# Kernel optimization log

Measured on AMD Instinct MI355X. Metric: run time of the kernel, lower is better.

## Reference

```python
import jax, jax.numpy as jnp
import numpy as np

N_NODES = 50000
N_EDGES = 800000
IN_FEAT = 4
HIDDEN = 128
NUM_LAYERS = 3


def setup_inputs() -> dict:
    key = jax.random.key(0)
    ks = jax.random.split(key, 16)
    x = jax.random.normal(ks[0], (N_NODES, IN_FEAT), dtype=jnp.float32)
    edge_index = jax.random.randint(ks[1], (2, N_EDGES), 0, N_NODES, dtype=jnp.int64)

    def lin(k, fan_in, fan_out):
        bound = 1.0 / np.sqrt(fan_in)
        k1, k2 = jax.random.split(k)
        W = jax.random.uniform(k1, (fan_in, fan_out), minval=-bound, maxval=bound, dtype=jnp.float32)
        b = jax.random.uniform(k2, (fan_out,), minval=-bound, maxval=bound, dtype=jnp.float32)
        return W, b

    W_enc, b_enc = lin(ks[2], IN_FEAT, HIDDEN)
    W_g1, b_g1 = lin(ks[3], HIDDEN, HIDDEN)
    W_g2, b_g2 = lin(ks[4], HIDDEN, HIDDEN)
    W_g3, b_g3 = lin(ks[5], HIDDEN, HIDDEN)
    W_m1, b_m1 = lin(ks[6], 2 * HIDDEN, HIDDEN)
    W_m2, b_m2 = lin(ks[7], HIDDEN, 3)
    return {
        "x": x, "edge_index": edge_index,
        "W_enc": W_enc, "b_enc": b_enc,
        "W_g1": W_g1, "b_g1": b_g1,
        "W_g2": W_g2, "b_g2": b_g2,
        "W_g3": W_g3, "b_g3": b_g3,
        "W_m1": W_m1, "b_m1": b_m1,
        "W_m2": W_m2, "b_m2": b_m2,
    }


def _gcn_forward(x, edge_index, W_enc, b_enc, gcn_params, W_m1, b_m1, W_m2, b_m2):
    n = x.shape[0]
    # Node encoder (linear + ReLU) -> [N, H]
    h = jax.nn.relu(x @ W_enc + b_enc)

    # Add self-loops once (GCNConv default add_self_loops=True)
    src = jnp.concatenate([edge_index[0], jnp.arange(n, dtype=edge_index.dtype)])
    dst = jnp.concatenate([edge_index[1], jnp.arange(n, dtype=edge_index.dtype)])
    # Symmetric degree normalization: D^{-1/2} (A+I) D^{-1/2}
    deg = jax.ops.segment_sum(jnp.ones_like(dst, dtype=h.dtype), dst, num_segments=n)
    deg_inv_sqrt = jnp.where(deg > 0, jax.lax.rsqrt(jnp.maximum(deg, 1.0)), 0.0)
    norm = (deg_inv_sqrt[src] * deg_inv_sqrt[dst])[:, None]  # [E+N, 1]

    for (W, b) in gcn_params:
        m = (h @ W)[src] * norm                       # gather + scale messages
        h = jax.ops.segment_sum(m, dst, num_segments=n) + b
        h = jax.nn.relu(h)                            # dropout is identity at eval

    # Edge classifier: gather endpoints, concat, MLP -> [E, 3]
    ef = jnp.concatenate([h[edge_index[0]], h[edge_index[1]]], axis=-1)
    return jax.nn.relu(ef @ W_m1 + b_m1) @ W_m2 + b_m2


def reference(x, edge_index, W_enc, b_enc, W_g1, b_g1, W_g2, b_g2, W_g3, b_g3, W_m1, b_m1, W_m2, b_m2):
    gcn_params = [(W_g1, b_g1), (W_g2, b_g2), (W_g3, b_g3)]
    return _gcn_forward(x, edge_index, W_enc, b_enc, gcn_params, W_m1, b_m1, W_m2, b_m2)
```

## Files before the change

kernel.cpp:

```cpp
#include <hip/hip_runtime.h>
#include <hip/hip_bf16.h>

#define N_NODES 50000
#define N_EDGES 800000
#define HID 128
#define NBUCKET 1024
#define N_NODE_BLOCKS ((N_NODES + 255) / 256)

typedef __attribute__((ext_vector_type(8))) short bf16x8;
typedef __attribute__((ext_vector_type(4))) float f32x4;

__device__ __forceinline__ ushort f2bf(float f) {
    uint u = __float_as_uint(f);
    return (ushort)((u + 0x7FFFu + ((u >> 16) & 1u)) >> 16);
}
__device__ __forceinline__ float bf2f(ushort h) { return __uint_as_float(((uint)h) << 16); }

__global__ void k_count(const int* __restrict__ ei, int* cnt) {
    int e = blockIdx.x * blockDim.x + threadIdx.x;
    if (e < N_EDGES) atomicAdd(&cnt[ei[N_EDGES + e]], 1);
}

__global__ __launch_bounds__(256) void k_bhist(const int* __restrict__ cnt, int* gHist,
                                               int* __restrict__ blockBase) {
    __shared__ int lh[NBUCKET];
    int t = threadIdx.x;
    for (int d = t; d < NBUCKET; d += 256) lh[d] = 0;
    __syncthreads();
    int n = blockIdx.x * 256 + t;
    if (n < N_NODES) {
        int deg = min(cnt[n], NBUCKET - 1);
        atomicAdd(&lh[deg], 1);
    }
    __syncthreads();
    for (int d = t; d < NBUCKET; d += 256) {
        int c = lh[d];
        blockBase[blockIdx.x * NBUCKET + d] = c ? atomicAdd(&gHist[d], c) : 0;
    }
}

__global__ __launch_bounds__(NBUCKET) void k_prefix(const int* __restrict__ gHist,
                                                    int* __restrict__ histBase,
                                                    int* __restrict__ edgeBase,
                                                    int* __restrict__ rowStartP) {
    __shared__ int a[NBUCKET];
    __shared__ int b[NBUCKET];
    int t = threadIdx.x;
    int h = gHist[t];
    a[t] = h;
    b[t] = h * t;
    __syncthreads();
    for (int off = 1; off < NBUCKET; off <<= 1) {
        int av = (t >= off) ? a[t - off] : 0;
        int bv = (t >= off) ? b[t - off] : 0;
        __syncthreads();
        a[t] += av;
        b[t] += bv;
        __syncthreads();
    }
    histBase[t] = a[t] - h;
    edgeBase[t] = b[t] - h * t;
    if (t == 0) rowStartP[N_NODES] = N_EDGES;
}

__global__ __launch_bounds__(256) void k_rank(const int* __restrict__ cnt,
                                              const int* __restrict__ histBase,
                                              const int* __restrict__ edgeBase,
                                              const int* __restrict__ blockBase,
                                              int* __restrict__ rank,
                                              int* __restrict__ rowStartP,
                                              float* __restrict__ dinvP) {
    __shared__ int cur[NBUCKET];
    int t = threadIdx.x;
    for (int d = t; d < NBUCKET; d += 256) cur[d] = 0;
    __syncthreads();
    int n = blockIdx.x * 256 + t;
    if (n < N_NODES) {
        int deg = min(cnt[n], NBUCKET - 1);
        int slot = atomicAdd(&cur[deg], 1);
        int r = histBase[deg] + blockBase[blockIdx.x * NBUCKET + deg] + slot;
        rank[n] = r;
        rowStartP[r] = edgeBase[deg] + (r - histBase[deg]) * deg;
        dinvP[r] = rsqrtf(1.0f + (float)deg);
    }
}

__global__ void k_fill(const int* __restrict__ ei, const int* __restrict__ rank,
                       const int* __restrict__ rowStartP, int* cursorP,
                       int2* __restrict__ csrE) {
    int e = blockIdx.x * blockDim.x + threadIdx.x;
    if (e < N_EDGES) {
        int s = ei[e];
        int d = ei[N_EDGES + e];
        int rd = rank[d];
        int pos = rowStartP[rd] + atomicAdd(&cursorP[rd], 1);
        csrE[pos] = make_int2(rank[s], e);
    }
}

struct WSplitArgs {
    const float* src[5];
    ushort* th[5];
    ushort* tl[5];
};

__global__ void k_tsplit5(WSplitArgs a) {
    int i = blockIdx.x * 256 + threadIdx.x;
    int which = i >> 14, r = i & 16383;
    int k = r >> 7, j = r & 127;
    float v = a.src[which][r];
    ushort hi = f2bf(v);
    a.th[which][j * 128 + k] = hi;
    a.tl[which][j * 128 + k] = f2bf(v - bf2f(hi));
}

__global__ void k_encoder(const float* __restrict__ x, const float* __restrict__ W,
                          const float* __restrict__ b, const int* __restrict__ rank,
                          ushort* __restrict__ hH, ushort* __restrict__ hL) {
    int i = blockIdx.x * 256 + threadIdx.x;
    int n = i >> 6, l = i & 63;
    int j = l * 2;
    float4 xv = *(const float4*)(x + (size_t)n * 4);
    float2 acc = *(const float2*)(b + j);
    float2 w0 = *(const float2*)(W + 0 * 128 + j);
    float2 w1 = *(const float2*)(W + 1 * 128 + j);
    float2 w2 = *(const float2*)(W + 2 * 128 + j);
    float2 w3 = *(const float2*)(W + 3 * 128 + j);
    acc.x += xv.x * w0.x + xv.y * w1.x + xv.z * w2.x + xv.w * w3.x;
    acc.y += xv.x * w0.y + xv.y * w1.y + xv.z * w2.y + xv.w * w3.y;
    float v0 = fmaxf(acc.x, 0.f), v1 = fmaxf(acc.y, 0.f);
    ushort h0 = f2bf(v0), h1 = f2bf(v1);
    ushort l0 = f2bf(v0 - bf2f(h0)), l1 = f2bf(v1 - bf2f(h1));
    size_t o = (size_t)rank[n] * 64 + l;
    ((uint*)hH)[o] = (uint)h0 | ((uint)h1 << 16);
    ((uint*)hL)[o] = (uint)l0 | ((uint)l1 << 16);
}

__global__ __launch_bounds__(256) void k_gemm_mfma(const ushort* __restrict__ AH,
                                                   const ushort* __restrict__ AL,
                                                   const ushort* __restrict__ BTH,
                                                   const ushort* __restrict__ BTL,
                                                   float* __restrict__ out,
                                                   const float* __restrict__ scale, int M) {
    int tid = threadIdx.x;
    int w = tid >> 6, l = tid & 63;
    int ln = l & 15, lk = l >> 4;
    int r0 = blockIdx.x * 128 + w * 32;
    int row0 = r0 + ln, row1 = r0 + 16 + ln;
    int a0 = row0 < M ? row0 : M - 1;
    int a1 = row1 < M ? row1 : M - 1;

    f32x4 acc0[8] = {};
    f32x4 acc1[8] = {};
#pragma unroll
    for (int kc = 0; kc < 4; ++kc) {
        int ko = kc * 32 + lk * 8;
        bf16x8 h0H = *(const bf16x8*)(AH + (size_t)a0 * 128 + ko);
        bf16x8 h0L = *(const bf16x8*)(AL + (size_t)a0 * 128 + ko);
        bf16x8 h1H = *(const bf16x8*)(AH + (size_t)a1 * 128 + ko);
        bf16x8 h1L = *(const bf16x8*)(AL + (size_t)a1 * 128 + ko);
#pragma unroll
        for (int nt = 0; nt < 8; ++nt) {
            size_t boff = (size_t)(nt * 16 + ln) * 128 + ko;
            bf16x8 wH = *(const bf16x8*)(BTH + boff);
            bf16x8 wL = *(const bf16x8*)(BTL + boff);
            acc0[nt] = __builtin_amdgcn_mfma_f32_16x16x32_bf16(wH, h0H, acc0[nt], 0, 0, 0);
            acc0[nt] = __builtin_amdgcn_mfma_f32_16x16x32_bf16(wL, h0H, acc0[nt], 0, 0, 0);
            acc0[nt] = __builtin_amdgcn_mfma_f32_16x16x32_bf16(wH, h0L, acc0[nt], 0, 0, 0);
            acc1[nt] = __builtin_amdgcn_mfma_f32_16x16x32_bf16(wH, h1H, acc1[nt], 0, 0, 0);
            acc1[nt] = __builtin_amdgcn_mfma_f32_16x16x32_bf16(wL, h1H, acc1[nt], 0, 0, 0);
            acc1[nt] = __builtin_amdgcn_mfma_f32_16x16x32_bf16(wH, h1L, acc1[nt], 0, 0, 0);
        }
    }
    float s0v = scale[a0];
    float s1v = scale[a1];
#pragma unroll
    for (int nt = 0; nt < 8; ++nt) {
        int jb = nt * 16 + lk * 4;
        if (row0 < M) {
            *(float4*)(out + (size_t)row0 * 128 + jb) =
                make_float4(acc0[nt][0] * s0v, acc0[nt][1] * s0v, acc0[nt][2] * s0v, acc0[nt][3] * s0v);
        }
        if (row1 < M) {
            *(float4*)(out + (size_t)row1 * 128 + jb) =
                make_float4(acc1[nt][0] * s1v, acc1[nt][1] * s1v, acc1[nt][2] * s1v, acc1[nt][3] * s1v);
        }
    }
}

__global__ __launch_bounds__(512, 8) void k_agg_gemm(
    const float* __restrict__ hw, const float* __restrict__ bg,
    const float* __restrict__ dinvP, const int* __restrict__ rowStartP,
    const int2* __restrict__ csrE,
    const ushort* __restrict__ BTH1, const ushort* __restrict__ BTL1,
    const ushort* __restrict__ BTH2, const ushort* __restrict__ BTL2,
    float* __restrict__ out1, float* __restrict__ out2,
    const float* __restrict__ b1, const float* __restrict__ outScale) {
    __shared__ uint AsH[16][68];
    __shared__ uint AsL[16][68];
    int tid = threadIdx.x;
    int w = tid >> 6, l = tid & 63;
    int sub = l >> 5;
    int g2 = (l >> 4) & 1;
    int li = l & 15;
    int c8 = li * 8;
    int n = blockIdx.x * 16 + w * 2 + sub;

    float4 aA, aB;
    if (g2 == 0) {
        aA = *(const float4*)(hw + (size_t)n * 128 + c8);
        aB = *(const float4*)(hw + (size_t)n * 128 + c8 + 4);
    } else {
        aA = make_float4(0.f, 0.f, 0.f, 0.f);
        aB = aA;
    }
    int s0 = rowStartP[n], s1 = rowStartP[n + 1];
    int k = s0 + g2;
    float4 v0a = make_float4(0.f, 0.f, 0.f, 0.f), v0b = v0a;
    if (k < s1) {
        const float* r = hw + (size_t)csrE[k].x * 128 + c8;
        v0a = *(const float4*)(r);
        v0b = *(const float4*)(r + 4);
    }
    for (; k < s1; k += 2) {
        float4 v1a = make_float4(0.f, 0.f, 0.f, 0.f), v1b = v1a;
        if (k + 2 < s1) {
            const float* r = hw + (size_t)csrE[k + 2].x * 128 + c8;
            v1a = *(const float4*)(r);
            v1b = *(const float4*)(r + 4);
        }
        aA.x += v0a.x; aA.y += v0a.y; aA.z += v0a.z; aA.w += v0a.w;
        aB.x += v0b.x; aB.y += v0b.y; aB.z += v0b.z; aB.w += v0b.w;
        v0a = v1a;
        v0b = v1b;
    }
    aA.x += __shfl_xor(aA.x, 16); aA.y += __shfl_xor(aA.y, 16);
    aA.z += __shfl_xor(aA.z, 16); aA.w += __shfl_xor(aA.w, 16);
    aB.x += __shfl_xor(aB.x, 16); aB.y += __shfl_xor(aB.y, 16);
    aB.z += __shfl_xor(aB.z, 16); aB.w += __shfl_xor(aB.w, 16);

    if (g2 == 0) {
        float di = dinvP[n];
        float4 bbA = *(const float4*)(bg + c8);
        float4 bbB = *(const float4*)(bg + c8 + 4);
        float f0 = fmaxf(bbA.x + di * aA.x, 0.f);
        float f1 = fmaxf(bbA.y + di * aA.y, 0.f);
        float f2 = fmaxf(bbA.z + di * aA.z, 0.f);
        float f3 = fmaxf(bbA.w + di * aA.w, 0.f);
        float f4 = fmaxf(bbB.x + di * aB.x, 0.f);
        float f5 = fmaxf(bbB.y + di * aB.y, 0.f);
        float f6 = fmaxf(bbB.z + di * aB.z, 0.f);
        float f7 = fmaxf(bbB.w + di * aB.w, 0.f);
        ushort h0 = f2bf(f0), h1 = f2bf(f1), h2 = f2bf(f2), h3 = f2bf(f3);
        ushort h4 = f2bf(f4), h5 = f2bf(f5), h6 = f2bf(f6), h7 = f2bf(f7);
        uint4 uh = make_uint4((uint)h0 | ((uint)h1 << 16), (uint)h2 | ((uint)h3 << 16),
                              (uint)h4 | ((uint)h5 << 16), (uint)h6 | ((uint)h7 << 16));
        ushort l0 = f2bf(f0 - bf2f(h0)), l1 = f2bf(f1 - bf2f(h1));
        ushort l2 = f2bf(f2 - bf2f(h2)), l3 = f2bf(f3 - bf2f(h3));
        ushort l4 = f2bf(f4 - bf2f(h4)), l5 = f2bf(f5 - bf2f(h5));
        ushort l6 = f2bf(f6 - bf2f(h6)), l7 = f2bf(f7 - bf2f(h7));
        uint4 ul = make_uint4((uint)l0 | ((uint)l1 << 16), (uint)l2 | ((uint)l3 << 16),
                              (uint)l4 | ((uint)l5 << 16), (uint)l6 | ((uint)l7 << 16));
        int r = w * 2 + sub;
        *(uint4*)&AsH[r][li * 4] = uh;
        *(uint4*)&AsL[r][li * 4] = ul;
    }
    __syncthreads();

    int ln = l & 15, lk = l >> 4;
    int ct = w;
    int node = blockIdx.x * 16 + ln;
    f32x4 acc1 = {};
    f32x4 acc2 = {};
#pragma unroll
    for (int kc = 0; kc < 4; ++kc) {
        uint4 uh = *(uint4*)&AsH[ln][kc * 16 + lk * 4];
        uint4 ul = *(uint4*)&AsL[ln][kc * 16 + lk * 4];
        bf16x8 hh, hl;
        __builtin_memcpy(&hh, &uh, 16);
        __builtin_memcpy(&hl, &ul, 16);
        size_t boff = (size_t)(ct * 16 + ln) * 128 + kc * 32 + lk * 8;
        bf16x8 wh = *(const bf16x8*)(BTH1 + boff);
        bf16x8 wl = *(const bf16x8*)(BTL1 + boff);
        acc1 = __builtin_amdgcn_mfma_f32_16x16x32_bf16(wh, hh, acc1, 0, 0, 0);
        acc1 = __builtin_amdgcn_mfma_f32_16x16x32_bf16(wl, hh, acc1, 0, 0, 0);
        acc1 = __builtin_amdgcn_mfma_f32_16x16x32_bf16(wh, hl, acc1, 0, 0, 0);
        if (BTH2) {
            bf16x8 wh2 = *(const bf16x8*)(BTH2 + boff);
            bf16x8 wl2 = *(const bf16x8*)(BTL2 + boff);
            acc2 = __builtin_amdgcn_mfma_f32_16x16x32_bf16(wh2, hh, acc2, 0, 0, 0);
            acc2 = __builtin_amdgcn_mfma_f32_16x16x32_bf16(wl2, hh, acc2, 0, 0, 0);
            acc2 = __builtin_amdgcn_mfma_f32_16x16x32_bf16(wh2, hl, acc2, 0, 0, 0);
        }
    }
    int jb = ct * 16 + lk * 4;
    if (outScale) {
        float s = outScale[node];
        *(float4*)(out1 + (size_t)node * 128 + jb) =
            make_float4(acc1[0] * s, acc1[1] * s, acc1[2] * s, acc1[3] * s);
    } else {
        *(float4*)(out1 + (size_t)node * 128 + jb) =
            make_float4(acc1[0], acc1[1], acc1[2], acc1[3]);
        float4 bv = *(const float4*)(b1 + jb);
        *(float4*)(out2 + (size_t)node * 128 + jb) =
            make_float4(acc2[0] + bv.x, acc2[1] + bv.y, acc2[2] + bv.z, acc2[3] + bv.w);
    }
}

__global__ __launch_bounds__(256) void k_edge_final(const float* __restrict__ P,
                                                    const float* __restrict__ Qb,
                                                    const int* __restrict__ rowStartP,
                                                    const int2* __restrict__ csrE,
                                                    const float* __restrict__ W2,
                                                    const float* __restrict__ b2,
                                                    float* __restrict__ out) {
    int wid = (blockIdx.x * 256 + threadIdx.x) >> 6;
    int l = threadIdx.x & 63;
    if (wid >= N_NODES) return;
    int s0 = rowStartP[wid], s1 = rowStartP[wid + 1];
    if (s0 >= s1) return;
    int j8 = (l & 15) * 8;
    int g = l >> 4;

    float4 qa = *(const float4*)(Qb + (size_t)wid * 128 + j8);
    float4 qb = *(const float4*)(Qb + (size_t)wid * 128 + j8 + 4);
    float w2r[8][3];
#pragma unroll
    for (int k = 0; k < 8; ++k) {
        w2r[k][0] = W2[(j8 + k) * 3 + 0];
        w2r[k][1] = W2[(j8 + k) * 3 + 1];
        w2r[k][2] = W2[(j8 + k) * 3 + 2];
    }
    float bz0 = b2[0], bz1 = b2[1], bz2 = b2[2];

    int k = s0 + g;
    int2 c = make_int2(0, 0);
    float4 pa = make_float4(0.f, 0.f, 0.f, 0.f), pb = pa;
    if (k < s1) {
        c = csrE[k];
        const float* pr = P + (size_t)c.x * 128 + j8;
        pa = *(const float4*)(pr);
        pb = *(const float4*)(pr + 4);
    }
    for (; k < s1; k += 4) {
        int kn = k + 4;
        int2 cn = make_int2(0, 0);
        float4 pan = make_float4(0.f, 0.f, 0.f, 0.f), pbn = pan;
        if (kn < s1) {
            cn = csrE[kn];
            const float* prn = P + (size_t)cn.x * 128 + j8;
            pan = *(const float4*)(prn);
            pbn = *(const float4*)(prn + 4);
        }
        float z[8];
        z[0] = fmaxf(pa.x + qa.x, 0.f);
        z[1] = fmaxf(pa.y + qa.y, 0.f);
        z[2] = fmaxf(pa.z + qa.z, 0.f);
        z[3] = fmaxf(pa.w + qa.w, 0.f);
        z[4] = fmaxf(pb.x + qb.x, 0.f);
        z[5] = fmaxf(pb.y + qb.y, 0.f);
        z[6] = fmaxf(pb.z + qb.z, 0.f);
        z[7] = fmaxf(pb.w + qb.w, 0.f);
        float o0 = 0.f, o1 = 0.f, o2 = 0.f;
#pragma unroll
        for (int q = 0; q < 8; ++q) {
            o0 += z[q] * w2r[q][0];
            o1 += z[q] * w2r[q][1];
            o2 += z[q] * w2r[q][2];
        }
#pragma unroll
        for (int m = 1; m < 16; m <<= 1) {
            o0 += __shfl_xor(o0, m);
            o1 += __shfl_xor(o1, m);
            o2 += __shfl_xor(o2, m);
        }
        if ((l & 15) == 0) {
            float* op = out + (size_t)c.y * 3;
            op[0] = o0 + bz0;
            op[1] = o1 + bz1;
            op[2] = o2 + bz2;
        }
        c = cn;
        pa = pan;
        pb = pbn;
    }
}

extern "C" void kernel_launch(void* const* d_in, const int* in_sizes, int n_in,
                              void* d_out, int out_size, void* d_ws, size_t ws_size,
                              hipStream_t stream) {
    const float* x     = (const float*)d_in[0];
    const int*   ei    = (const int*)d_in[1];
    const float* W_enc = (const float*)d_in[2];
    const float* b_enc = (const float*)d_in[3];
    const float* Wg[3] = {(const float*)d_in[4], (const float*)d_in[6], (const float*)d_in[8]};
    const float* bg[3] = {(const float*)d_in[5], (const float*)d_in[7], (const float*)d_in[9]};
    const float* W_m1  = (const float*)d_in[10];
    const float* b_m1  = (const float*)d_in[11];
    const float* W_m2  = (const float*)d_in[12];
    const float* b_m2  = (const float*)d_in[13];
    float* out = (float*)d_out;

    char* w = (char*)d_ws;
    ushort* hH      = (ushort*)w;  w += (size_t)N_NODES * HID * 2;
    ushort* hL      = (ushort*)w;  w += (size_t)N_NODES * HID * 2;
    float*  bufA    = (float*)w;   w += (size_t)N_NODES * HID * 4;
    float*  bufB    = (float*)w;   w += (size_t)N_NODES * HID * 4;
    int2*   csrE    = (int2*)w;    w += (size_t)N_EDGES * 8;
    int*    cnt     = (int*)w;     w += (size_t)N_NODES * 4;
    int*    cursorP = (int*)w;     w += (size_t)N_NODES * 4;
    int*    gHist   = (int*)w;     w += NBUCKET * 4;
    size_t  zeroBytes = (size_t)(N_NODES * 2 + NBUCKET) * 4;
    int*    rank    = (int*)w;     w += (size_t)N_NODES * 4;
    int*    rowStartP = (int*)w;   w += (size_t)(N_NODES + 4) * 4;
    float*  dinvP   = (float*)w;   w += (size_t)N_NODES * 4;
    int*    histBase = (int*)w;    w += NBUCKET * 4;
    int*    edgeBase = (int*)w;    w += NBUCKET * 4;
    int*    blockBase = (int*)w;   w += (size_t)N_NODE_BLOCKS * NBUCKET * 4;
    ushort* WgTH[3], *WgTL[3];
    for (int i = 0; i < 3; ++i) {
        WgTH[i] = (ushort*)w; w += 128 * 128 * 2;
        WgTL[i] = (ushort*)w; w += 128 * 128 * 2;
    }
    ushort* WtTH = (ushort*)w; w += 128 * 128 * 2;
    ushort* WtTL = (ushort*)w; w += 128 * 128 * 2;
    ushort* WbTH = (ushort*)w; w += 128 * 128 * 2;
    ushort* WbTL = (ushort*)w; w += 128 * 128 * 2;

    float* P  = (float*)hH;
    float* Qb = bufB;

    hipMemsetAsync(cnt, 0, zeroBytes, stream);
    k_count<<<(N_EDGES + 255) / 256, 256, 0, stream>>>(ei, cnt);
    k_bhist<<<N_NODE_BLOCKS, 256, 0, stream>>>(cnt, gHist, blockBase);
    k_prefix<<<1, NBUCKET, 0, stream>>>(gHist, histBase, edgeBase, rowStartP);
    k_rank<<<N_NODE_BLOCKS, 256, 0, stream>>>(cnt, histBase, edgeBase, blockBase,
                                              rank, rowStartP, dinvP);
    k_fill<<<(N_EDGES + 255) / 256, 256, 0, stream>>>(ei, rank, rowStartP, cursorP, csrE);

    WSplitArgs wa;
    wa.src[0] = Wg[0]; wa.th[0] = WgTH[0]; wa.tl[0] = WgTL[0];
    wa.src[1] = Wg[1]; wa.th[1] = WgTH[1]; wa.tl[1] = WgTL[1];
    wa.src[2] = Wg[2]; wa.th[2] = WgTH[2]; wa.tl[2] = WgTL[2];
    wa.src[3] = W_m1;             wa.th[3] = WtTH; wa.tl[3] = WtTL;
    wa.src[4] = W_m1 + 128 * 128; wa.th[4] = WbTH; wa.tl[4] = WbTL;
    k_tsplit5<<<5 * 16384 / 256, 256, 0, stream>>>(wa);

    k_encoder<<<N_NODES * 64 / 256, 256, 0, stream>>>(x, W_enc, b_enc, rank, hH, hL);

    k_gemm_mfma<<<(N_NODES + 127) / 128, 256, 0, stream>>>(hH, hL, WgTH[0], WgTL[0],
                                                           bufA, dinvP, N_NODES);

    const int fusedGrid = N_NODES / 16;
    k_agg_gemm<<<fusedGrid, 512, 0, stream>>>(bufA, bg[0], dinvP, rowStartP, csrE,
                                              WgTH[1], WgTL[1], nullptr, nullptr,
                                              bufB, nullptr, nullptr, dinvP);
    k_agg_gemm<<<fusedGrid, 512, 0, stream>>>(bufB, bg[1], dinvP, rowStartP, csrE,
                                              WgTH[2], WgTL[2], nullptr, nullptr,
                                              bufA, nullptr, nullptr, dinvP);
    k_agg_gemm<<<fusedGrid, 512, 0, stream>>>(bufA, bg[2], dinvP, rowStartP, csrE,
                                              WtTH, WtTL, WbTH, WbTL,
                                              P, Qb, b_m1, nullptr);

    k_edge_final<<<(N_NODES * 64) / 256, 256, 0, stream>>>(P, Qb, rowStartP, csrE,
                                                           W_m2, b_m2, out);
}
```

Baseline: 456.8 us.

## Use one wave per node for aggregation and split dual GEMM across waves

Fused aggregate+GEMM blocks grow from 512 to 1024 threads. Each wave now aggregates one node with four neighbor groups instead of two nodes per wave, using an extra shuffle reduction across 32 lanes. In the final layer, the two output GEMMs (P and Qb) go to separate halves of the waves instead of one wave computing both. The aim is more memory-level parallelism in the gather and a shorter serial MFMA chain per wave. The cost is larger blocks with lower occupancy hints, and idle waves in the first two layers where the second-half waves return early.

```diff
diff --git a/kernel.cpp b/kernel.cpp
--- a/kernel.cpp
+++ b/kernel.cpp
@@ -188,7 +188,7 @@
     }
 }
 
-__global__ __launch_bounds__(512, 8) void k_agg_gemm(
+__global__ __launch_bounds__(1024, 2) void k_agg_gemm(
     const float* __restrict__ hw, const float* __restrict__ bg,
     const float* __restrict__ dinvP, const int* __restrict__ rowStartP,
     const int2* __restrict__ csrE,
@@ -200,14 +200,12 @@
     __shared__ uint AsL[16][68];
     int tid = threadIdx.x;
     int w = tid >> 6, l = tid & 63;
-    int sub = l >> 5;
-    int g2 = (l >> 4) & 1;
-    int li = l & 15;
+    int g = l >> 4, li = l & 15;
     int c8 = li * 8;
-    int n = blockIdx.x * 16 + w * 2 + sub;
+    int n = blockIdx.x * 16 + w;
 
     float4 aA, aB;
-    if (g2 == 0) {
+    if (g == 0) {
         aA = *(const float4*)(hw + (size_t)n * 128 + c8);
         aB = *(const float4*)(hw + (size_t)n * 128 + c8 + 4);
     } else {
@@ -215,17 +213,17 @@
         aB = aA;
     }
     int s0 = rowStartP[n], s1 = rowStartP[n + 1];
-    int k = s0 + g2;
+    int k = s0 + g;
     float4 v0a = make_float4(0.f, 0.f, 0.f, 0.f), v0b = v0a;
     if (k < s1) {
         const float* r = hw + (size_t)csrE[k].x * 128 + c8;
         v0a = *(const float4*)(r);
         v0b = *(const float4*)(r + 4);
     }
-    for (; k < s1; k += 2) {
+    for (; k < s1; k += 4) {
         float4 v1a = make_float4(0.f, 0.f, 0.f, 0.f), v1b = v1a;
-        if (k + 2 < s1) {
-            const float* r = hw + (size_t)csrE[k + 2].x * 128 + c8;
+        if (k + 4 < s1) {
+            const float* r = hw + (size_t)csrE[k + 4].x * 128 + c8;
             v1a = *(const float4*)(r);
             v1b = *(const float4*)(r + 4);
         }
@@ -238,8 +236,12 @@
     aA.z += __shfl_xor(aA.z, 16); aA.w += __shfl_xor(aA.w, 16);
     aB.x += __shfl_xor(aB.x, 16); aB.y += __shfl_xor(aB.y, 16);
     aB.z += __shfl_xor(aB.z, 16); aB.w += __shfl_xor(aB.w, 16);
-
-    if (g2 == 0) {
+    aA.x += __shfl_xor(aA.x, 32); aA.y += __shfl_xor(aA.y, 32);
+    aA.z += __shfl_xor(aA.z, 32); aA.w += __shfl_xor(aA.w, 32);
+    aB.x += __shfl_xor(aB.x, 32); aB.y += __shfl_xor(aB.y, 32);
+    aB.z += __shfl_xor(aB.z, 32); aB.w += __shfl_xor(aB.w, 32);
+
+    if (g == 0) {
         float di = dinvP[n];
         float4 bbA = *(const float4*)(bg + c8);
         float4 bbB = *(const float4*)(bg + c8 + 4);
@@ -261,17 +263,19 @@
         ushort l6 = f2bf(f6 - bf2f(h6)), l7 = f2bf(f7 - bf2f(h7));
         uint4 ul = make_uint4((uint)l0 | ((uint)l1 << 16), (uint)l2 | ((uint)l3 << 16),
                               (uint)l4 | ((uint)l5 << 16), (uint)l6 | ((uint)l7 << 16));
-        int r = w * 2 + sub;
-        *(uint4*)&AsH[r][li * 4] = uh;
-        *(uint4*)&AsL[r][li * 4] = ul;
+        *(uint4*)&AsH[w][li * 4] = uh;
+        *(uint4*)&AsL[w][li * 4] = ul;
     }
     __syncthreads();
 
+    bool second = w >= 8;
+    if (second && !BTH2) return;
+    const ushort* TH = second ? BTH2 : BTH1;
+    const ushort* TL = second ? BTL2 : BTL1;
     int ln = l & 15, lk = l >> 4;
-    int ct = w;
+    int ct = w & 7;
     int node = blockIdx.x * 16 + ln;
-    f32x4 acc1 = {};
-    f32x4 acc2 = {};
+    f32x4 acc = {};
 #pragma unroll
     for (int kc = 0; kc < 4; ++kc) {
         uint4 uh = *(uint4*)&AsH[ln][kc * 16 + lk * 4];
@@ -280,30 +284,24 @@
         __builtin_memcpy(&hh, &uh, 16);
         __builtin_memcpy(&hl, &ul, 16);
         size_t boff = (size_t)(ct * 16 + ln) * 128 + kc * 32 + lk * 8;
-        bf16x8 wh = *(const bf16x8*)(BTH1 + boff);
-        bf16x8 wl = *(const bf16x8*)(BTL1 + boff);
-        acc1 = __builtin_amdgcn_mfma_f32_16x16x32_bf16(wh, hh, acc1, 0, 0, 0);
-        acc1 = __builtin_amdgcn_mfma_f32_16x16x32_bf16(wl, hh, acc1, 0, 0, 0);
-        acc1 = __builtin_amdgcn_mfma_f32_16x16x32_bf16(wh, hl, acc1, 0, 0, 0);
-        if (BTH2) {
-            bf16x8 wh2 = *(const bf16x8*)(BTH2 + boff);
-            bf16x8 wl2 = *(const bf16x8*)(BTL2 + boff);
-            acc2 = __builtin_amdgcn_mfma_f32_16x16x32_bf16(wh2, hh, acc2, 0, 0, 0);
-            acc2 = __builtin_amdgcn_mfma_f32_16x16x32_bf16(wl2, hh, acc2, 0, 0, 0);
-            acc2 = __builtin_amdgcn_mfma_f32_16x16x32_bf16(wh2, hl, acc2, 0, 0, 0);
-        }
+        bf16x8 wh = *(const bf16x8*)(TH + boff);
+        bf16x8 wl = *(const bf16x8*)(TL + boff);
+        acc = __builtin_amdgcn_mfma_f32_16x16x32_bf16(wh, hh, acc, 0, 0, 0);
+        acc = __builtin_amdgcn_mfma_f32_16x16x32_bf16(wl, hh, acc, 0, 0, 0);
+        acc = __builtin_amdgcn_mfma_f32_16x16x32_bf16(wh, hl, acc, 0, 0, 0);
     }
     int jb = ct * 16 + lk * 4;
     if (outScale) {
         float s = outScale[node];
         *(float4*)(out1 + (size_t)node * 128 + jb) =
-            make_float4(acc1[0] * s, acc1[1] * s, acc1[2] * s, acc1[3] * s);
+            make_float4(acc[0] * s, acc[1] * s, acc[2] * s, acc[3] * s);
+    } else if (!second) {
+        *(float4*)(out1 + (size_t)node * 128 + jb) =
+            make_float4(acc[0], acc[1], acc[2], acc[3]);
     } else {
-        *(float4*)(out1 + (size_t)node * 128 + jb) =
-            make_float4(acc1[0], acc1[1], acc1[2], acc1[3]);
         float4 bv = *(const float4*)(b1 + jb);
         *(float4*)(out2 + (size_t)node * 128 + jb) =
-            make_float4(acc2[0] + bv.x, acc2[1] + bv.y, acc2[2] + bv.z, acc2[3] + bv.w);
+            make_float4(acc[0] + bv.x, acc[1] + bv.y, acc[2] + bv.z, acc[3] + bv.w);
     }
 }
 
@@ -452,15 +450,15 @@
                                                            bufA, dinvP, N_NODES);
 
     const int fusedGrid = N_NODES / 16;
-    k_agg_gemm<<<fusedGrid, 512, 0, stream>>>(bufA, bg[0], dinvP, rowStartP, csrE,
-                                              WgTH[1], WgTL[1], nullptr, nullptr,
-                                              bufB, nullptr, nullptr, dinvP);
-    k_agg_gemm<<<fusedGrid, 512, 0, stream>>>(bufB, bg[1], dinvP, rowStartP, csrE,
-                                              WgTH[2], WgTL[2], nullptr, nullptr,
-                                              bufA, nullptr, nullptr, dinvP);
-    k_agg_gemm<<<fusedGrid, 512, 0, stream>>>(bufA, bg[2], dinvP, rowStartP, csrE,
-                                              WtTH, WtTL, WbTH, WbTL,
-                                              P, Qb, b_m1, nullptr);
+    k_agg_gemm<<<fusedGrid, 1024, 0, stream>>>(bufA, bg[0], dinvP, rowStartP, csrE,
+                                               WgTH[1], WgTL[1], nullptr, nullptr,
+                                               bufB, nullptr, nullptr, dinvP);
+    k_agg_gemm<<<fusedGrid, 1024, 0, stream>>>(bufB, bg[1], dinvP, rowStartP, csrE,
+                                               WgTH[2], WgTL[2], nullptr, nullptr,
+                                               bufA, nullptr, nullptr, dinvP);
+    k_agg_gemm<<<fusedGrid, 1024, 0, stream>>>(bufA, bg[2], dinvP, rowStartP, csrE,
+                                               WtTH, WtTL, WbTH, WbTL,
+                                               P, Qb, b_m1, nullptr);
 
     k_edge_final<<<(N_NODES * 64) / 256, 256, 0, stream>>>(P, Qb, rowStartP, csrE,
                                                            W_m2, b_m2, out);
```

After: 467.4 us. 1.02x slower.
